# Kernel optimization log

Measured on AMD Instinct MI355X. Metric: run time of the kernel, lower is better.

## Reference

```python
import jax, jax.numpy as jnp
import numpy as np

N_NODES = 50000
N_EDGES = 1_000_000
D_IN = 64
HID = 64
N_GRAPHS = 128


def setup_inputs() -> dict:
    key = jax.random.key(0)
    ks = jax.random.split(key, 12)
    s = 1.0 / np.sqrt(HID)
    x = jax.random.normal(ks[0], (N_NODES, D_IN), dtype=jnp.float32)
    edge_index = jax.random.randint(ks[1], (2, N_EDGES), 0, N_NODES, dtype=jnp.int32)
    # every graph id occupied, sorted (like PyG batch vector)
    batch_index = (jnp.arange(N_NODES, dtype=jnp.int32) * N_GRAPHS) // N_NODES
    return {
        "x": x,
        "Wl0": jax.random.normal(ks[2], (HID, D_IN), jnp.float32) * s,
        "Wr0": jax.random.normal(ks[3], (HID, D_IN), jnp.float32) * s,
        "bl0": jax.random.normal(ks[4], (HID,), jnp.float32) * s,
        "Wl": jax.random.normal(ks[5], (HID, HID), jnp.float32) * s,
        "Wr": jax.random.normal(ks[6], (HID, HID), jnp.float32) * s,
        "bl": jax.random.normal(ks[7], (HID,), jnp.float32) * s,
        "W1": jax.random.normal(ks[8], (HID, HID), jnp.float32) * s,
        "b1": jax.random.normal(ks[9], (HID,), jnp.float32) * s,
        "W2": jax.random.normal(ks[10], (3, HID), jnp.float32) * s,
        "b2": jax.random.normal(ks[11], (3,), jnp.float32) * s,
        "edge_index": edge_index,
        "batch_index": batch_index,
    }


def _sage_conv(x, Wl, Wr, bl, src, dst, n_nodes):
    # PyG SAGEConv (aggr='mean'): out = lin_l(mean_{j in N(i)} x_j) + lin_r(x_i)
    msgs = jnp.take(x, src, axis=0)                               # [E, D] gather
    agg = jax.ops.segment_sum(msgs, dst, num_segments=n_nodes)    # [N, D] scatter-add
    deg = jax.ops.segment_sum(jnp.ones((src.shape[0],), x.dtype), dst, num_segments=n_nodes)
    mean = agg / jnp.clip(deg, 1.0)[:, None]
    return mean @ Wl.T + bl + x @ Wr.T


def reference(x, Wl0, Wr0, bl0, Wl, Wr, bl, W1, b1, W2, b2, edge_index, batch_index):
    src, dst = edge_index[0], edge_index[1]
    n = x.shape[0]
    h = jnp.tanh(_sage_conv(x, Wl0, Wr0, bl0, src, dst, n))
    # same SAGEConv instance reused 3 times
    for _ in range(3):
        h = jnp.tanh(_sage_conv(h, Wl, Wr, bl, src, dst, n))
    pooled = jax.ops.segment_max(h, batch_index, num_segments=N_GRAPHS)  # [G, H]
    # same lin1 reused 3 times
    g = pooled
    for _ in range(3):
        g = jnp.tanh(g @ W1.T + b1)
    return g @ W2.T + b2
```

## Files before the change

### kernel.cpp

```cpp
#include <hip/hip_runtime.h>
#include <math.h>

#define NT 256
#define NTS 128

typedef unsigned short ushort_t;
typedef unsigned int uint_t;
typedef __attribute__((ext_vector_type(8))) short bf16x8;
typedef __attribute__((ext_vector_type(4))) float f32x4;

__device__ __forceinline__ int rli(int v, int l) {
    return __builtin_amdgcn_readlane(v, l);
}
__device__ __forceinline__ int imax(int a, int b) { return a > b ? a : b; }
__device__ __forceinline__ int imin(int a, int b) { return a < b ? a : b; }

__device__ __forceinline__ ushort_t f2bf_rne(float f) {
    uint_t u = __float_as_uint(f);
    uint_t r = u + 0x7FFF + ((u >> 16) & 1);
    return (ushort_t)(r >> 16);
}
__device__ __forceinline__ float bf2f(ushort_t b) {
    return __uint_as_float(((uint_t)b) << 16);
}
__device__ __forceinline__ float rlf(float v, int l) {
    return __int_as_float(__builtin_amdgcn_readlane(__float_as_int(v), l));
}


__global__ void zero_i32(int* __restrict__ p, int n) {
    int t = blockIdx.x * blockDim.x + threadIdx.x;
    if (t < n) p[t] = 0;
}

__global__ void hist_dst(int* __restrict__ cnt, const int* __restrict__ dst, int n_edges) {
    int e = blockIdx.x * blockDim.x + threadIdx.x;
    if (e < n_edges) atomicAdd(&cnt[dst[e]], 1);
}

__global__ void scan_blocks(const int* __restrict__ cnt, int* __restrict__ bsum, int n) {
    __shared__ int s[NT];
    int i = blockIdx.x * NT + threadIdx.x;
    s[threadIdx.x] = (i < n) ? cnt[i] : 0;
    __syncthreads();
    for (int off = NT / 2; off > 0; off >>= 1) {
        if (threadIdx.x < off) s[threadIdx.x] += s[threadIdx.x + off];
        __syncthreads();
    }
    if (threadIdx.x == 0) bsum[blockIdx.x] = s[0];
}

__global__ void scan_bsum(const int* __restrict__ bsum, int* __restrict__ boff,
                          int nb, int* __restrict__ row_off, int n) {
    __shared__ int s[1024];
    int tid = threadIdx.x;
    int v = (tid < nb) ? bsum[tid] : 0;
    s[tid] = v;
    __syncthreads();
    for (int off = 1; off < 1024; off <<= 1) {
        int t = (tid >= off) ? s[tid - off] : 0;
        __syncthreads();
        s[tid] += t;
        __syncthreads();
    }
    if (tid < nb) boff[tid] = s[tid] - v;
    if (tid == nb - 1) row_off[n] = s[tid];
}

__global__ void scan_final(const int* __restrict__ cnt, const int* __restrict__ boff,
                           int* __restrict__ row_off, int* __restrict__ cursor, int n) {
    __shared__ int s[NT];
    int i = blockIdx.x * NT + threadIdx.x;
    int v = (i < n) ? cnt[i] : 0;
    s[threadIdx.x] = v;
    __syncthreads();
    for (int off = 1; off < NT; off <<= 1) {
        int t = (threadIdx.x >= off) ? s[threadIdx.x - off] : 0;
        __syncthreads();
        s[threadIdx.x] += t;
        __syncthreads();
    }
    if (i < n) {
        int ex = boff[blockIdx.x] + s[threadIdx.x] - v;
        row_off[i] = ex;
        cursor[i] = ex;
    }
}

__global__ void edge_scatter(int* __restrict__ csr_src, int* __restrict__ cursor,
                             const int* __restrict__ src, const int* __restrict__ dst,
                             int n_edges) {
    int e = blockIdx.x * blockDim.x + threadIdx.x;
    if (e < n_edges) {
        int p = atomicAdd(&cursor[dst[e]], 1);
        csr_src[p] = src[e];
    }
}


__global__ void f2bf_kern(ushort_t* __restrict__ o, const float* __restrict__ in, int n) {
    int t = blockIdx.x * blockDim.x + threadIdx.x;
    if (t < n) o[t] = f2bf_rne(in[t]);
}

__global__ void pack_w(ushort_t* __restrict__ packed, const float* __restrict__ Wl,
                       const float* __restrict__ Wr) {
    int t = blockIdx.x * blockDim.x + threadIdx.x;
    if (t < 8192) {
        int i = t & 7;
        int lane = (t >> 3) & 63;
        int nt = (t >> 9) & 3;
        int ks = t >> 11;
        int k = ks * 32 + ((lane >> 4) << 3) + i;
        int f = nt * 16 + (lane & 15);
        float w = (k < 64) ? Wl[f * 64 + k] : Wr[f * 64 + (k - 64)];
        packed[t] = f2bf_rne(w);
    }
}


__global__ void pool_init(float* __restrict__ pooled, int n) {
    int t = blockIdx.x * blockDim.x + threadIdx.x;
    if (t < n) pooled[t] = -INFINITY;
}

__device__ __forceinline__ void atomicMaxFloat(float* addr, float value) {
    if (value >= 0.0f)
        atomicMax((int*)addr, __float_as_int(value));
    else
        atomicMin((unsigned int*)addr, (unsigned int)__float_as_int(value));
}

__global__ __launch_bounds__(NTS, 8) void sage_layer(
    ushort_t* __restrict__ out_bf, float* __restrict__ pooled,
    const ushort_t* __restrict__ hb_in,
    const int* __restrict__ row_off, const int* __restrict__ csr_src,
    const int* __restrict__ batch,
    const ushort_t* __restrict__ pw,
    const float* __restrict__ bl,
    int n_nodes, int do_pool) {
    __shared__ ushort_t A[16 * 136];
    int tid = threadIdx.x;
    int lane = tid & 63;
    int v = tid >> 6;
    int g0 = blockIdx.x * 16 + v * 8;
    int l31 = lane & 31;
    int h = lane >> 5;
    const uint_t* hb32 = (const uint_t*)hb_in;

    int roidx = imin(g0 + imin(lane, 8), n_nodes);
    int ro = row_off[roidx];

#pragma unroll
    for (int n = 0; n < 8; ++n) {
        int g = g0 + n;
        int row = v * 8 + n;
        int b = rli(ro, n);
        int e_ = rli(ro, n + 1);
        int d = e_ - b;
        bool ok = g < n_nodes;

        A[row * 136 + 64 + lane] = ok ? hb_in[((size_t)g << 6) + lane] : (ushort_t)0;

        if (ok && d <= 64) {
            int idx = csr_src[b + (lane < d ? lane : imax(d - 1, 0))];
            float accLo = 0.f, accHi = 0.f;
            for (int jj = 0; jj < d; jj += 16) {
                uint_t w0, w1, w2, w3, w4, w5, w6, w7;
#define LD(L, W)                                                              \
                {                                                             \
                    int eA = imin(jj + 2 * (L), d - 1);                       \
                    int eB = imin(jj + 2 * (L) + 1, d - 1);                   \
                    int iA = rli(idx, eA);                                    \
                    int iB = rli(idx, eB);                                    \
                    int is = (lane < 32) ? iA : iB;                           \
                    W = hb32[((size_t)(unsigned)is << 5) + l31];              \
                }
                LD(0, w0) LD(1, w1) LD(2, w2) LD(3, w3)
                LD(4, w4) LD(5, w5) LD(6, w6) LD(7, w7)
#undef LD
#define CS(L, W)                                                              \
                {                                                             \
                    float f = ((jj + 2 * (L) + h) < d) ? 1.f : 0.f;           \
                    accLo += f * __uint_as_float((W) << 16);                  \
                    accHi += f * __uint_as_float((W) & 0xffff0000u);          \
                }
                CS(0, w0) CS(1, w1) CS(2, w2) CS(3, w3)
                CS(4, w4) CS(5, w5) CS(6, w6) CS(7, w7)
#undef CS
            }
            accLo += __shfl_xor(accLo, 32);
            accHi += __shfl_xor(accHi, 32);
            float inv = 1.0f / (float)imax(d, 1);
            if (lane < 32) {
                uint_t mw = (uint_t)f2bf_rne(accLo * inv) |
                            ((uint_t)f2bf_rne(accHi * inv) << 16);
                *(uint_t*)&A[row * 136 + 2 * l31] = mw;
            }
        } else if (ok) {
            float aa = 0.f;
            for (int cb = b; cb < e_; cb += 64) {
                int m = e_ - cb; if (m > 64) m = 64;
                int lidx = cb + (lane < m ? lane : m - 1);
                int idx2 = csr_src[lidx];
                for (int j = 0; j < m; ++j)
                    aa += bf2f(hb_in[((size_t)(unsigned)rli(idx2, j) << 6) + lane]);
            }
            A[row * 136 + lane] = f2bf_rne(aa * (1.0f / (float)imax(d, 1)));
        } else {
            A[row * 136 + lane] = 0;
        }
    }
    __syncthreads();

    int a_row = lane & 15;
    int kbase = (lane >> 4) << 3;
#pragma unroll
    for (int p = 0; p < 2; ++p) {
        int nt = v * 2 + p;
        f32x4 acc = {0.f, 0.f, 0.f, 0.f};
#pragma unroll
        for (int ks = 0; ks < 4; ++ks) {
            bf16x8 af = *reinterpret_cast<const bf16x8*>(&A[a_row * 136 + ks * 32 + kbase]);
            bf16x8 bf = *reinterpret_cast<const bf16x8*>(&pw[(((ks << 2) + nt) * 64 + lane) << 3]);
            acc = __builtin_amdgcn_mfma_f32_16x16x32_bf16(af, bf, acc, 0, 0, 0);
        }
        int c = nt * 16 + (lane & 15);
        float bias = bl[c];
        int rbase = blockIdx.x * 16 + ((lane >> 4) << 2);
#pragma unroll
        for (int j = 0; j < 4; ++j) {
            int g = rbase + j;
            if (g < n_nodes) {
                float o = tanhf(acc[j] + bias);
                if (do_pool) {
                    atomicMaxFloat(&pooled[(size_t)batch[g] * 64 + c], o);
                } else {
                    out_bf[(size_t)g * 64 + c] = f2bf_rne(o);
                }
            }
        }
    }
}

__global__ void head(float* __restrict__ out, const float* __restrict__ pooled,
                     const float* __restrict__ W1, const float* __restrict__ b1,
                     const float* __restrict__ W2, const float* __restrict__ b2) {
    __shared__ float W1T[64][64];
    int tid = threadIdx.x;
    for (int t = tid; t < 4096; t += NT) {
        int f = t >> 6, k = t & 63;
        W1T[k][f] = W1[t];
    }
    __syncthreads();

    int lane = tid & 63;
    int g = blockIdx.x * (NT >> 6) + (tid >> 6);
    float v = pooled[(size_t)g * 64 + lane];
    float bias = b1[lane];
#pragma unroll
    for (int it = 0; it < 3; ++it) {
        float acc = bias;
#pragma unroll
        for (int k = 0; k < 64; ++k) {
            acc += rlf(v, k) * W1T[k][lane];
        }
        v = tanhf(acc);
    }
#pragma unroll
    for (int j = 0; j < 3; ++j) {
        float p = v * W2[j * 64 + lane];
#pragma unroll
        for (int off = 32; off >= 1; off >>= 1) p += __shfl_xor(p, off);
        if (lane == 0) out[g * 3 + j] = p + b2[j];
    }
}


extern "C" void kernel_launch(void* const* d_in, const int* in_sizes, int n_in,
                              void* d_out, int out_size, void* d_ws, size_t ws_size,
                              hipStream_t stream) {
    const float* x   = (const float*)d_in[0];
    const float* Wl0 = (const float*)d_in[1];
    const float* Wr0 = (const float*)d_in[2];
    const float* bl0 = (const float*)d_in[3];
    const float* Wl  = (const float*)d_in[4];
    const float* Wr  = (const float*)d_in[5];
    const float* bl  = (const float*)d_in[6];
    const float* W1  = (const float*)d_in[7];
    const float* b1  = (const float*)d_in[8];
    const float* W2  = (const float*)d_in[9];
    const float* b2  = (const float*)d_in[10];
    const int* ei    = (const int*)d_in[11];
    const int* batch = (const int*)d_in[12];

    int n_nodes = in_sizes[0] / 64;
    int n_edges = in_sizes[11] / 2;
    const int* src = ei;
    const int* dst = ei + n_edges;

    int nb = (n_nodes + NT - 1) / NT;
    size_t nfeat = (size_t)n_nodes * 64;

    int* csr_src  = (int*)d_ws;
    int* row_off  = csr_src + n_edges;
    int* cursor   = row_off + (n_nodes + 1);
    int* cnt      = cursor + n_nodes;
    int* bsum     = cnt + n_nodes;
    int* boff     = bsum + nb;
    float* pooled = (float*)(boff + nb);
    ushort_t* pw0 = (ushort_t*)(pooled + 128 * 64);
    ushort_t* pw  = pw0 + 8192;
    ushort_t* bfX = pw + 8192;
    ushort_t* bfA = bfX + nfeat;
    ushort_t* bfB = bfA + nfeat;

    int eblk = (n_edges + NT - 1) / NT;
    int sage_blk = (n_nodes + 15) / 16;

    zero_i32<<<nb, NT, 0, stream>>>(cnt, n_nodes);
    hist_dst<<<eblk, NT, 0, stream>>>(cnt, dst, n_edges);
    scan_blocks<<<nb, NT, 0, stream>>>(cnt, bsum, n_nodes);
    scan_bsum<<<1, 1024, 0, stream>>>(bsum, boff, nb, row_off, n_nodes);
    scan_final<<<nb, NT, 0, stream>>>(cnt, boff, row_off, cursor, n_nodes);
    edge_scatter<<<eblk, NT, 0, stream>>>(csr_src, cursor, src, dst, n_edges);

    f2bf_kern<<<(int)((nfeat + NT - 1) / NT), NT, 0, stream>>>(bfX, x, (int)nfeat);
    pack_w<<<32, NT, 0, stream>>>(pw0, Wl0, Wr0);
    pack_w<<<32, NT, 0, stream>>>(pw, Wl, Wr);
    pool_init<<<(128 * 64 + NT - 1) / NT, NT, 0, stream>>>(pooled, 128 * 64);

    sage_layer<<<sage_blk, NTS, 0, stream>>>(bfA, pooled, bfX, row_off, csr_src,
                                             batch, pw0, bl0, n_nodes, 0);
    sage_layer<<<sage_blk, NTS, 0, stream>>>(bfB, pooled, bfA, row_off, csr_src,
                                             batch, pw, bl, n_nodes, 0);
    sage_layer<<<sage_blk, NTS, 0, stream>>>(bfA, pooled, bfB, row_off, csr_src,
                                             batch, pw, bl, n_nodes, 0);
    sage_layer<<<sage_blk, NTS, 0, stream>>>(bfB, pooled, bfA, row_off, csr_src,
                                             batch, pw, bl, n_nodes, 1);

    head<<<32, NT, 0, stream>>>((float*)d_out, pooled, W1, b1, W2, b2);
}
```

Measured before the change: 399.7 us.

## Widen neighbor gather to 8-byte loads, hoist index loads, fuse prep kernels

Each neighbor row is now gathered by 16 lanes with 8-byte loads, so one wave covers four neighbors per load instead of two, with four accumulators and a two-step shuffle reduction. The CSR index loads and self-feature loads for all eight nodes are hoisted ahead of the per-node gathers to expose more memory-level parallelism. The four small preprocessing kernels are merged into one grid-stride prep kernel to cut launch overhead. Hoisting raises register pressure, which may reduce occupancy under the launch bounds.

```diff
diff --git a/kernel.cpp b/kernel.cpp
--- a/kernel.cpp
+++ b/kernel.cpp
@@ -97,38 +97,103 @@
     }
 }
 
-
-__global__ void f2bf_kern(ushort_t* __restrict__ o, const float* __restrict__ in, int n) {
-    int t = blockIdx.x * blockDim.x + threadIdx.x;
-    if (t < n) o[t] = f2bf_rne(in[t]);
-}
-
-__global__ void pack_w(ushort_t* __restrict__ packed, const float* __restrict__ Wl,
-                       const float* __restrict__ Wr) {
-    int t = blockIdx.x * blockDim.x + threadIdx.x;
-    if (t < 8192) {
-        int i = t & 7;
-        int lane = (t >> 3) & 63;
-        int nt = (t >> 9) & 3;
-        int ks = t >> 11;
-        int k = ks * 32 + ((lane >> 4) << 3) + i;
-        int f = nt * 16 + (lane & 15);
-        float w = (k < 64) ? Wl[f * 64 + k] : Wr[f * 64 + (k - 64)];
-        packed[t] = f2bf_rne(w);
-    }
-}
-
-
-__global__ void pool_init(float* __restrict__ pooled, int n) {
-    int t = blockIdx.x * blockDim.x + threadIdx.x;
-    if (t < n) pooled[t] = -INFINITY;
-}
+__device__ __forceinline__ ushort_t pack_one(int t, const float* Wl, const float* Wr) {
+    int i = t & 7;
+    int lane = (t >> 3) & 63;
+    int nt = (t >> 9) & 3;
+    int ks = t >> 11;
+    int k = ks * 32 + ((lane >> 4) << 3) + i;
+    int f = nt * 16 + (lane & 15);
+    float w = (k < 64) ? Wl[f * 64 + k] : Wr[f * 64 + (k - 64)];
+    return f2bf_rne(w);
+}
+
+__global__ void prep(ushort_t* __restrict__ bfX, const float* __restrict__ x, int nfeat,
+                     ushort_t* __restrict__ pw0, const float* __restrict__ Wl0,
+                     const float* __restrict__ Wr0,
+                     ushort_t* __restrict__ pw, const float* __restrict__ Wl,
+                     const float* __restrict__ Wr,
+                     float* __restrict__ pooled) {
+    int t = blockIdx.x * NT + threadIdx.x;
+    int stride = gridDim.x * NT;
+    for (int i = t; i < nfeat; i += stride) bfX[i] = f2bf_rne(x[i]);
+    for (int i = t; i < 8192; i += stride) {
+        pw0[i] = pack_one(i, Wl0, Wr0);
+        pw[i] = pack_one(i, Wl, Wr);
+        pooled[i] = -INFINITY;
+    }
+}
+
 
 __device__ __forceinline__ void atomicMaxFloat(float* addr, float value) {
     if (value >= 0.0f)
         atomicMax((int*)addr, __float_as_int(value));
     else
         atomicMin((unsigned int*)addr, (unsigned int)__float_as_int(value));
+}
+
+__device__ __forceinline__ void gather_node(
+    ushort_t* __restrict__ A, int row, bool ok, int idx, int b, int d,
+    const uint2* __restrict__ hb8, const ushort_t* __restrict__ hb_in,
+    const int* __restrict__ csr_src, int lane, int l15, int q) {
+    int dm1 = imax(d - 1, 0);
+    if (ok && d <= 64) {
+        float a0 = 0.f, a1 = 0.f, a2 = 0.f, a3 = 0.f;
+        for (int jj = 0; jj < d; jj += 32) {
+            uint2 w0, w1, w2, w3, w4, w5, w6, w7;
+#define LD(L, W)                                                              \
+            {                                                                 \
+                int p0 = imin(jj + 4 * (L) + 0, dm1);                         \
+                int p1 = imin(jj + 4 * (L) + 1, dm1);                         \
+                int p2 = imin(jj + 4 * (L) + 2, dm1);                         \
+                int p3 = imin(jj + 4 * (L) + 3, dm1);                         \
+                int r0 = rli(idx, p0), r1 = rli(idx, p1);                     \
+                int r2 = rli(idx, p2), r3 = rli(idx, p3);                     \
+                int is = q < 2 ? (q == 0 ? r0 : r1) : (q == 2 ? r2 : r3);     \
+                W = hb8[((size_t)(unsigned)is << 4) + l15];                   \
+            }
+            LD(0, w0) LD(1, w1) LD(2, w2) LD(3, w3)
+            LD(4, w4) LD(5, w5) LD(6, w6) LD(7, w7)
+#undef LD
+#define CS(L, W)                                                              \
+            {                                                                 \
+                float f = ((jj + 4 * (L) + q) < d) ? 1.f : 0.f;               \
+                a0 += f * __uint_as_float((W).x << 16);                       \
+                a1 += f * __uint_as_float((W).x & 0xffff0000u);               \
+                a2 += f * __uint_as_float((W).y << 16);                       \
+                a3 += f * __uint_as_float((W).y & 0xffff0000u);               \
+            }
+            CS(0, w0) CS(1, w1) CS(2, w2) CS(3, w3)
+            CS(4, w4) CS(5, w5) CS(6, w6) CS(7, w7)
+#undef CS
+        }
+        a0 += __shfl_xor(a0, 16); a0 += __shfl_xor(a0, 32);
+        a1 += __shfl_xor(a1, 16); a1 += __shfl_xor(a1, 32);
+        a2 += __shfl_xor(a2, 16); a2 += __shfl_xor(a2, 32);
+        a3 += __shfl_xor(a3, 16); a3 += __shfl_xor(a3, 32);
+        float inv = 1.0f / (float)imax(d, 1);
+        if (lane < 16) {
+            uint_t m0 = (uint_t)f2bf_rne(a0 * inv) |
+                        ((uint_t)f2bf_rne(a1 * inv) << 16);
+            uint_t m1 = (uint_t)f2bf_rne(a2 * inv) |
+                        ((uint_t)f2bf_rne(a3 * inv) << 16);
+            *(uint_t*)&A[row * 136 + 4 * l15] = m0;
+            *(uint_t*)&A[row * 136 + 4 * l15 + 2] = m1;
+        }
+    } else if (ok) {
+        float aa = 0.f;
+        int e_ = b + d;
+        for (int cb = b; cb < e_; cb += 64) {
+            int m = e_ - cb; if (m > 64) m = 64;
+            int lidx = cb + (lane < m ? lane : m - 1);
+            int idx2 = csr_src[lidx];
+            for (int j = 0; j < m; ++j)
+                aa += bf2f(hb_in[((size_t)(unsigned)rli(idx2, j) << 6) + lane]);
+        }
+        A[row * 136 + lane] = f2bf_rne(aa * (1.0f / (float)imax(d, 1)));
+    } else {
+        A[row * 136 + lane] = 0;
+    }
 }
 
 __global__ __launch_bounds__(NTS, 8) void sage_layer(
@@ -144,73 +209,46 @@
     int lane = tid & 63;
     int v = tid >> 6;
     int g0 = blockIdx.x * 16 + v * 8;
-    int l31 = lane & 31;
-    int h = lane >> 5;
-    const uint_t* hb32 = (const uint_t*)hb_in;
+    int l15 = lane & 15;
+    int q = lane >> 4;
+    const uint2* hb8 = (const uint2*)hb_in;
 
     int roidx = imin(g0 + imin(lane, 8), n_nodes);
     int ro = row_off[roidx];
 
-#pragma unroll
-    for (int n = 0; n < 8; ++n) {
-        int g = g0 + n;
-        int row = v * 8 + n;
-        int b = rli(ro, n);
-        int e_ = rli(ro, n + 1);
-        int d = e_ - b;
-        bool ok = g < n_nodes;
-
-        A[row * 136 + 64 + lane] = ok ? hb_in[((size_t)g << 6) + lane] : (ushort_t)0;
-
-        if (ok && d <= 64) {
-            int idx = csr_src[b + (lane < d ? lane : imax(d - 1, 0))];
-            float accLo = 0.f, accHi = 0.f;
-            for (int jj = 0; jj < d; jj += 16) {
-                uint_t w0, w1, w2, w3, w4, w5, w6, w7;
-#define LD(L, W)                                                              \
-                {                                                             \
-                    int eA = imin(jj + 2 * (L), d - 1);                       \
-                    int eB = imin(jj + 2 * (L) + 1, d - 1);                   \
-                    int iA = rli(idx, eA);                                    \
-                    int iB = rli(idx, eB);                                    \
-                    int is = (lane < 32) ? iA : iB;                           \
-                    W = hb32[((size_t)(unsigned)is << 5) + l31];              \
-                }
-                LD(0, w0) LD(1, w1) LD(2, w2) LD(3, w3)
-                LD(4, w4) LD(5, w5) LD(6, w6) LD(7, w7)
-#undef LD
-#define CS(L, W)                                                              \
-                {                                                             \
-                    float f = ((jj + 2 * (L) + h) < d) ? 1.f : 0.f;           \
-                    accLo += f * __uint_as_float((W) << 16);                  \
-                    accHi += f * __uint_as_float((W) & 0xffff0000u);          \
-                }
-                CS(0, w0) CS(1, w1) CS(2, w2) CS(3, w3)
-                CS(4, w4) CS(5, w5) CS(6, w6) CS(7, w7)
-#undef CS
-            }
-            accLo += __shfl_xor(accLo, 32);
-            accHi += __shfl_xor(accHi, 32);
-            float inv = 1.0f / (float)imax(d, 1);
-            if (lane < 32) {
-                uint_t mw = (uint_t)f2bf_rne(accLo * inv) |
-                            ((uint_t)f2bf_rne(accHi * inv) << 16);
-                *(uint_t*)&A[row * 136 + 2 * l31] = mw;
-            }
-        } else if (ok) {
-            float aa = 0.f;
-            for (int cb = b; cb < e_; cb += 64) {
-                int m = e_ - cb; if (m > 64) m = 64;
-                int lidx = cb + (lane < m ? lane : m - 1);
-                int idx2 = csr_src[lidx];
-                for (int j = 0; j < m; ++j)
-                    aa += bf2f(hb_in[((size_t)(unsigned)rli(idx2, j) << 6) + lane]);
-            }
-            A[row * 136 + lane] = f2bf_rne(aa * (1.0f / (float)imax(d, 1)));
-        } else {
-            A[row * 136 + lane] = 0;
-        }
-    }
+    int b0 = rli(ro, 0), b1 = rli(ro, 1), b2 = rli(ro, 2), b3 = rli(ro, 3);
+    int b4 = rli(ro, 4), b5 = rli(ro, 5), b6 = rli(ro, 6), b7 = rli(ro, 7);
+    int e8 = rli(ro, 8);
+    int d0 = b1 - b0, d1 = b2 - b1, d2 = b3 - b2, d3 = b4 - b3;
+    int d4 = b5 - b4, d5 = b6 - b5, d6 = b7 - b6, d7 = e8 - b7;
+
+#define IDXLD(N) int idx##N = csr_src[b##N + (lane < d##N ? lane : imax(d##N - 1, 0))];
+    IDXLD(0) IDXLD(1) IDXLD(2) IDXLD(3) IDXLD(4) IDXLD(5) IDXLD(6) IDXLD(7)
+#undef IDXLD
+#define HVLD(N) ushort_t hv##N = (g0 + (N) < n_nodes) \
+        ? hb_in[((size_t)(g0 + (N)) << 6) + lane] : (ushort_t)0;
+    HVLD(0) HVLD(1) HVLD(2) HVLD(3) HVLD(4) HVLD(5) HVLD(6) HVLD(7)
+#undef HVLD
+    {
+        int rb = v * 8;
+        A[(rb + 0) * 136 + 64 + lane] = hv0;
+        A[(rb + 1) * 136 + 64 + lane] = hv1;
+        A[(rb + 2) * 136 + 64 + lane] = hv2;
+        A[(rb + 3) * 136 + 64 + lane] = hv3;
+        A[(rb + 4) * 136 + 64 + lane] = hv4;
+        A[(rb + 5) * 136 + 64 + lane] = hv5;
+        A[(rb + 6) * 136 + 64 + lane] = hv6;
+        A[(rb + 7) * 136 + 64 + lane] = hv7;
+    }
+
+    gather_node(A, v * 8 + 0, g0 + 0 < n_nodes, idx0, b0, d0, hb8, hb_in, csr_src, lane, l15, q);
+    gather_node(A, v * 8 + 1, g0 + 1 < n_nodes, idx1, b1, d1, hb8, hb_in, csr_src, lane, l15, q);
+    gather_node(A, v * 8 + 2, g0 + 2 < n_nodes, idx2, b2, d2, hb8, hb_in, csr_src, lane, l15, q);
+    gather_node(A, v * 8 + 3, g0 + 3 < n_nodes, idx3, b3, d3, hb8, hb_in, csr_src, lane, l15, q);
+    gather_node(A, v * 8 + 4, g0 + 4 < n_nodes, idx4, b4, d4, hb8, hb_in, csr_src, lane, l15, q);
+    gather_node(A, v * 8 + 5, g0 + 5 < n_nodes, idx5, b5, d5, hb8, hb_in, csr_src, lane, l15, q);
+    gather_node(A, v * 8 + 6, g0 + 6 < n_nodes, idx6, b6, d6, hb8, hb_in, csr_src, lane, l15, q);
+    gather_node(A, v * 8 + 7, g0 + 7 < n_nodes, idx7, b7, d7, hb8, hb_in, csr_src, lane, l15, q);
     __syncthreads();
 
     int a_row = lane & 15;
@@ -325,10 +363,7 @@
     scan_final<<<nb, NT, 0, stream>>>(cnt, boff, row_off, cursor, n_nodes);
     edge_scatter<<<eblk, NT, 0, stream>>>(csr_src, cursor, src, dst, n_edges);
 
-    f2bf_kern<<<(int)((nfeat + NT - 1) / NT), NT, 0, stream>>>(bfX, x, (int)nfeat);
-    pack_w<<<32, NT, 0, stream>>>(pw0, Wl0, Wr0);
-    pack_w<<<32, NT, 0, stream>>>(pw, Wl, Wr);
-    pool_init<<<(128 * 64 + NT - 1) / NT, NT, 0, stream>>>(pooled, 128 * 64);
+    prep<<<1024, NT, 0, stream>>>(bfX, x, (int)nfeat, pw0, Wl0, Wr0, pw, Wl, Wr, pooled);
 
     sage_layer<<<sage_blk, NTS, 0, stream>>>(bfA, pooled, bfX, row_off, csr_src,
                                              batch, pw0, bl0, n_nodes, 0);
```

Result: faster. 383.6 us (-4.0%).
